# Kernel tuning notes

Hardware: AMD Instinct MI355X
Metric: run time of the kernel (lower is better)

Reference implementation:

```python
import jax, jax.numpy as jnp
import numpy as np
from jax import lax

N, CIN, COUT, H, W = 16, 512, 256, 32, 32
EPS = 1e-5


def _conv(x, w, b, pad_h, pad_w):
    # x: [N,Cin,H,W], w: [Cout,Cin,kh,kw], pad = ((top,bottom),(left,right))
    y = lax.conv_general_dilated(
        x, w, window_strides=(1, 1), padding=(pad_h, pad_w),
        dimension_numbers=("NCHW", "OIHW", "NCHW"))
    return y + b[None, :, None, None]


def setup_inputs() -> dict:
    key = jax.random.key(0)
    ks = jax.random.split(key, 12)
    s = 0.02
    return {
        "x": jax.random.normal(ks[0], (N, CIN, H, W), jnp.float32),
        "w1": jax.random.normal(ks[1], (COUT, CIN, 3, 3), jnp.float32) * s,
        "b1": jax.random.normal(ks[2], (COUT,), jnp.float32) * s,
        "w2": jax.random.normal(ks[3], (COUT, CIN, 2, 3), jnp.float32) * s,
        "b2": jax.random.normal(ks[4], (COUT,), jnp.float32) * s,
        "w3": jax.random.normal(ks[5], (COUT, CIN, 3, 2), jnp.float32) * s,
        "b3": jax.random.normal(ks[6], (COUT,), jnp.float32) * s,
        "w4": jax.random.normal(ks[7], (COUT, CIN, 2, 2), jnp.float32) * s,
        "b4": jax.random.normal(ks[8], (COUT,), jnp.float32) * s,
        "gamma": jnp.ones((COUT,), jnp.float32),
        "beta": jnp.zeros((COUT,), jnp.float32),
    }


def reference(x, w1, b1, w2, b2, w3, b3, w4, b4, gamma, beta):
    # torch F.pad(l,r,t,b) -> lax padding ((top,bottom),(left,right))
    o1 = _conv(x, w1, b1, (1, 1), (1, 1))  # 3x3, pad (1,1,1,1) -> [N,Cout,H,W]
    o2 = _conv(x, w2, b2, (1, 0), (1, 1))  # 2x3, pad (1,1,1,0)
    o3 = _conv(x, w3, b3, (1, 1), (1, 0))  # 3x2, pad (1,0,1,1)
    o4 = _conv(x, w4, b4, (1, 0), (1, 0))  # 2x2, pad (1,0,1,0)
    # pixel-shuffle interleave: o1->(even,even), o2->(odd,even), o3->(even,odd), o4->(odd,odd)
    row_even = jnp.stack([o1, o3], axis=-1).reshape(N, COUT, H, 2 * W)
    row_odd = jnp.stack([o2, o4], axis=-1).reshape(N, COUT, H, 2 * W)
    y = jnp.stack([row_even, row_odd], axis=-2).reshape(N, COUT, 2 * H, 2 * W)
    # BatchNorm2d, training mode: biased batch stats over (N,H,W)
    mean = jnp.mean(y, axis=(0, 2, 3), keepdims=True)
    var = jnp.mean(jnp.square(y - mean), axis=(0, 2, 3), keepdims=True)
    normed = (y - mean) * lax.rsqrt(var + EPS)
    normed = normed * gamma[None, :, None, None] + beta[None, :, None, None]
    return jax.nn.relu(normed)
```

## Files before the change

kernel.cpp:

```cpp
#include <hip/hip_runtime.h>
#include <hip/hip_bf16.h>


typedef unsigned short ushort_t;
typedef __attribute__((ext_vector_type(8))) short short8;
typedef __attribute__((ext_vector_type(4))) float floatx4;
typedef __attribute__((ext_vector_type(2))) float floatx2;
typedef __attribute__((ext_vector_type(4))) unsigned short u16x4;
typedef __attribute__((ext_vector_type(8))) unsigned short u16x8;
typedef __attribute__((ext_vector_type(4))) unsigned int u32x4;

#define XT_OFF    0u
#define WT_OFF    18939904u
#define BIAS_OFF  28377088u
#define STATS_OFF 28381184u

#define NSITES 204

#define ASYNC16(g, l) __builtin_amdgcn_global_load_lds( \
    (const __attribute__((address_space(1))) void*)(g), \
    (__attribute__((address_space(3))) void*)(l), 16, 0, 0)

__device__ __forceinline__ ushort_t f2bf(float f) {
  unsigned int u = __builtin_bit_cast(unsigned int, f);
  u += 0x7fffu + ((u >> 16) & 1u);
  return (ushort_t)(u >> 16);
}

__global__ __launch_bounds__(256) void prep_all(
    const float* __restrict__ x, ushort_t* __restrict__ xt,
    const float* __restrict__ w1, const float* __restrict__ w2,
    const float* __restrict__ w3, const float* __restrict__ w4,
    const float* __restrict__ b1, const float* __restrict__ b2,
    const float* __restrict__ b3, const float* __restrict__ b4,
    ushort_t* __restrict__ wt, float* __restrict__ bias,
    float* __restrict__ stats) {
  __shared__ ushort_t lds[128 * 36];
  const int t = threadIdx.x;
  if (blockIdx.x >= 544) {
    const int nout = blockIdx.x - 544;
    if (nout == 0 && t < 256) { stats[t] = 0.f; stats[256 + t] = 0.f; }
    const int q = nout >> 8, co = nout & 255;
    const int row = co * 4 + q;
    const float* wsrc; const float* bsrc; int khl, kwl;
    if (q == 0)      { wsrc = w1; bsrc = b1; khl = 3; kwl = 3; }
    else if (q == 1) { wsrc = w2; bsrc = b2; khl = 2; kwl = 3; }
    else if (q == 2) { wsrc = w3; bsrc = b3; khl = 3; kwl = 2; }
    else             { wsrc = w4; bsrc = b4; khl = 2; kwl = 2; }
    if (t == 0) bias[row] = bsrc[co];
    ushort_t* dst = wt + (size_t)row * 4608;
    for (int tap = 0; tap < 9; ++tap) {
      const int dh = tap / 3, dw = tap % 3;
      const bool valid = (dh < khl) && (dw < kwl);
#pragma unroll
      for (int cc = 0; cc < 2; ++cc) {
        const int ci = cc * 256 + t;
        ushort_t v = 0;
        if (valid)
          v = f2bf(wsrc[(((size_t)co * 512 + ci) * khl + dh) * kwl + dw]);
        dst[tap * 512 + ci] = v;
      }
    }
    return;
  }
  const int b = blockIdx.x;
  const int n = b / 34, hp = b % 34;
  ushort_t* dst = xt + (size_t)(n * 34 + hp) * (34 * 512);
  if (hp == 0 || hp == 33) {
    u32x4 z = {0u, 0u, 0u, 0u};
    for (int i = t; i < 2176; i += 256) ((u32x4*)dst)[i] = z;
    return;
  }
  const int h = hp - 1;
  {
    u32x4 z = {0u, 0u, 0u, 0u};
    if (t < 64) ((u32x4*)dst)[t] = z;
    else if (t < 128) ((u32x4*)(dst + 33 * 512))[t - 64] = z;
  }
  const size_t base = (size_t)n * 524288 + (size_t)h * 32;
  for (int ci0 = 0; ci0 < 512; ci0 += 128) {
    __syncthreads();
    {
      const int cil = t >> 3;
      const int w4 = (t & 7) << 2;
#pragma unroll
      for (int cc = 0; cc < 4; ++cc) {
        const int ci = cil + cc * 32;
        floatx4 v = *(const floatx4*)(x + base + (size_t)(ci0 + ci) * 1024 + w4);
        u16x4 hv;
#pragma unroll
        for (int j = 0; j < 4; ++j) hv[j] = f2bf(v[j]);
        *(u16x4*)&lds[ci * 36 + w4] = hv;
      }
    }
    __syncthreads();
    {
      const int w = t & 31;
      const int j8 = t >> 5;
#pragma unroll
      for (int cc2 = 0; cc2 < 2; ++cc2) {
        const int cil = cc2 * 64 + j8 * 8;
        u16x8 v;
#pragma unroll
        for (int j = 0; j < 8; ++j) v[j] = lds[(cil + j) * 36 + w];
        *(u16x8*)(dst + (w + 1) * 512 + ci0 + cil) = v;
      }
    }
  }
}

__global__ __launch_bounds__(256) void gemm_kernel(
    const ushort_t* __restrict__ xt, const ushort_t* __restrict__ wt,
    const float* __restrict__ bias, float* __restrict__ out,
    float* __restrict__ stats) {
  __shared__ char ldsX[NSITES * 128];
  __shared__ char ldsW[2][64 * 128];
  const int tid = threadIdx.x;
  const int bx = blockIdx.x;
  const int bn = bx & 15, bm = bx >> 4;
  const int n0 = bn << 6;
  const int n_img = bm >> 3;
  const int h0p = (bm & 7) << 2;
  const int wv = tid >> 6, lane = tid & 63;
  const int ri = lane & 15, kg = lane >> 4;
  const int wm = (wv & 1) << 6, wn = (wv >> 1) << 5;

  const char* xgp[7];
  char* xlp[7];
  {
    const char* xg = (const char*)(xt + (size_t)(n_img * 34 + h0p) * (34 * 512));
#pragma unroll
    for (int p = 0; p < 7; ++p) {
      const int idx = p * 256 + tid;
      const int site = idx >> 3, slot = idx & 7;
      const int c = slot ^ (site & 7);
      xgp[p] = xg + site * 1024 + (c << 4);
      xlp[p] = ldsX + idx * 16;
    }
  }
  const char* wgp[2];
  char* wlp0[2];
  char* wlp1[2];
#pragma unroll
  for (int p = 0; p < 2; ++p) {
    const int idx = p * 256 + tid;
    const int row = idx >> 3, slot = idx & 7;
    const int c = slot ^ (row & 7);
    wgp[p] = (const char*)wt + (size_t)(n0 + row) * 9216 + (c << 4);
    wlp0[p] = ldsW[0] + idx * 16;
    wlp1[p] = ldsW[1] + idx * 16;
  }

  floatx4 acc[2][4] = {};

  int arow[2], bsite[4];
#pragma unroll
  for (int f = 0; f < 2; ++f) arow[f] = wn + (f << 4) + ri;
#pragma unroll
  for (int fj = 0; fj < 4; ++fj)
    bsite[fj] = ((wm >> 5) + (fj >> 1)) * 34 + ((fj & 1) << 4) + ri;

  for (int chunk = 0; chunk < 8; ++chunk) {
    const int cb = chunk << 7;
#pragma unroll
    for (int p = 0; p < 6; ++p) ASYNC16(xgp[p] + cb, xlp[p]);
    if (tid < 96) ASYNC16(xgp[6] + cb, xlp[6]);
#pragma unroll
    for (int p = 0; p < 2; ++p) ASYNC16(wgp[p] + cb, wlp0[p]);
    __syncthreads();
#pragma unroll
    for (int tap = 0; tap < 9; ++tap) {
      if (tap < 8) {
        const int noff = ((tap + 1) << 10) + cb;
        if (tap & 1) {
#pragma unroll
          for (int p = 0; p < 2; ++p) ASYNC16(wgp[p] + noff, wlp0[p]);
        } else {
#pragma unroll
          for (int p = 0; p < 2; ++p) ASYNC16(wgp[p] + noff, wlp1[p]);
        }
      }
      const char* wb = ldsW[tap & 1];
      const int tapo = ((tap / 3) * 34 + (tap % 3)) * 128;
#pragma unroll
      for (int ks = 0; ks < 2; ++ks) {
        const int c = (ks << 2) + kg;
        short8 a4[2], b4[4];
#pragma unroll
        for (int f = 0; f < 2; ++f)
          a4[f] = *(const short8*)(wb + arow[f] * 128 +
                                   ((c ^ (arow[f] & 7)) << 4));
#pragma unroll
        for (int fj = 0; fj < 4; ++fj) {
          const int srow = bsite[fj] + (tap / 3) * 34 + (tap % 3);
          b4[fj] = *(const short8*)(ldsX + bsite[fj] * 128 + tapo +
                                    ((c ^ (srow & 7)) << 4));
        }
#pragma unroll
        for (int fi = 0; fi < 2; ++fi)
#pragma unroll
          for (int fj = 0; fj < 4; ++fj)
            acc[fi][fj] = __builtin_amdgcn_mfma_f32_16x16x32_bf16(
                a4[fi], b4[fj], acc[fi][fj], 0, 0, 0);
      }
      __syncthreads();
    }
  }

  const int quad = kg, colL = ri;
#pragma unroll
  for (int fi = 0; fi < 2; ++fi) {
    const int co = ((n0 + wn + (fi << 4)) >> 2) + quad;
    const floatx4 bv = *(const floatx4*)(bias + n0 + wn + (fi << 4) + (quad << 2));
    float s = 0.f, s2 = 0.f;
    float* obase = out + ((size_t)(n_img * 256 + co) << 12);
#pragma unroll
    for (int fj = 0; fj < 4; ++fj) {
      const int mb = wm + (fj << 4) + colL;
      const int hl = mb >> 5, w = mb & 31;
      const int h = h0p + hl;
      float v0 = acc[fi][fj][0] + bv[0];
      float v1 = acc[fi][fj][1] + bv[1];
      float v2 = acc[fi][fj][2] + bv[2];
      float v3 = acc[fi][fj][3] + bv[3];
      s += (v0 + v1) + (v2 + v3);
      s2 += v0 * v0 + v1 * v1 + v2 * v2 + v3 * v3;
      float* p = obase + (h << 7) + (w << 1);
      floatx2 e = {v0, v2};
      floatx2 o = {v1, v3};
      *(floatx2*)p = e;
      *(floatx2*)(p + 64) = o;
    }
#pragma unroll
    for (int off = 1; off < 16; off <<= 1) {
      s += __shfl_xor(s, off);
      s2 += __shfl_xor(s2, off);
    }
    if (colL == 0) {
      atomicAdd(&stats[co], s);
      atomicAdd(&stats[256 + co], s2);
    }
  }
}

__global__ __launch_bounds__(256) void bn_apply(
    float* __restrict__ y, const float* __restrict__ stats,
    const float* __restrict__ gamma, const float* __restrict__ beta) {
  const int b = blockIdx.x;
  const int co = b & 255;
  const int t = threadIdx.x;
  const float mean = stats[co] * (1.f / 65536.f);
  const float var = stats[256 + co] * (1.f / 65536.f) - mean * mean;
  const float rstd = rsqrtf(var + 1e-5f);
  const float scale = rstd * gamma[co];
  const float shift = beta[co] - mean * scale;
  float* p = y + (size_t)b * 4096;
#pragma unroll
  for (int it = 0; it < 4; ++it) {
    floatx4* q = (floatx4*)(p + (it * 256 + t) * 4);
    floatx4 v = *q;
#pragma unroll
    for (int e = 0; e < 4; ++e) v[e] = fmaxf(v[e] * scale + shift, 0.f);
    *q = v;
  }
}

extern "C" void kernel_launch(void* const* d_in, const int* in_sizes, int n_in,
                              void* d_out, int out_size, void* d_ws,
                              size_t ws_size, hipStream_t stream) {
  const float* x  = (const float*)d_in[0];
  const float* w1 = (const float*)d_in[1];
  const float* b1 = (const float*)d_in[2];
  const float* w2 = (const float*)d_in[3];
  const float* b2 = (const float*)d_in[4];
  const float* w3 = (const float*)d_in[5];
  const float* b3 = (const float*)d_in[6];
  const float* w4 = (const float*)d_in[7];
  const float* b4 = (const float*)d_in[8];
  const float* gamma = (const float*)d_in[9];
  const float* beta  = (const float*)d_in[10];
  float* out = (float*)d_out;

  char* ws = (char*)d_ws;
  ushort_t* xt   = (ushort_t*)(ws + XT_OFF);
  ushort_t* wt   = (ushort_t*)(ws + WT_OFF);
  float*    bias = (float*)(ws + BIAS_OFF);
  float*    st   = (float*)(ws + STATS_OFF);

  prep_all<<<544 + 1024, 256, 0, stream>>>(x, xt, w1, w2, w3, w4,
                                           b1, b2, b3, b4, wt, bias, st);
  gemm_kernel<<<2048, 256, 0, stream>>>(xt, wt, bias, out, st);
  bn_apply<<<4096, 256, 0, stream>>>(out, st, gamma, beta);
}
```

Measured before the change: 286.3 us.

## Load weights straight to registers in MFMA fragment layout and double N tile

The weight matrix is now pre-permuted into a panel layout that matches the MFMA A-fragment order. Each lane loads its fragments directly from global memory into a register double buffer, which removes the LDS staging of weights and the per-tap barrier. The block tile along N is doubled from 64 to 128, so each block holds a 4x4 fragment accumulator set and the grid is halved. This raises reuse of the staged X data, but it increases register pressure from 16 accumulators plus 16 u32x4 buffers, and it relies on global or L2 latency being hidden by prefetching one tap ahead.

```diff
diff --git a/kernel.cpp b/kernel.cpp
--- a/kernel.cpp
+++ b/kernel.cpp
@@ -16,6 +16,11 @@
 #define STATS_OFF 28381184u
 
 #define NSITES 204
+
+#define W_KS   8192
+#define W_TAP  16384
+#define W_CHK  147456
+#define W_PAN  1179648
 
 #define ASYNC16(g, l) __builtin_amdgcn_global_load_lds( \
     (const __attribute__((address_space(1))) void*)(g), \
@@ -42,13 +47,14 @@
     if (nout == 0 && t < 256) { stats[t] = 0.f; stats[256 + t] = 0.f; }
     const int q = nout >> 8, co = nout & 255;
     const int row = co * 4 + q;
+    const int panel = row >> 7, g = (row & 127) >> 4, riw = row & 15;
     const float* wsrc; const float* bsrc; int khl, kwl;
     if (q == 0)      { wsrc = w1; bsrc = b1; khl = 3; kwl = 3; }
     else if (q == 1) { wsrc = w2; bsrc = b2; khl = 2; kwl = 3; }
     else if (q == 2) { wsrc = w3; bsrc = b3; khl = 3; kwl = 2; }
     else             { wsrc = w4; bsrc = b4; khl = 2; kwl = 2; }
     if (t == 0) bias[row] = bsrc[co];
-    ushort_t* dst = wt + (size_t)row * 4608;
+    ushort_t* dstp = wt + (size_t)panel * (W_PAN / 2) + g * 512 + riw * 8;
     for (int tap = 0; tap < 9; ++tap) {
       const int dh = tap / 3, dw = tap % 3;
       const bool valid = (dh < khl) && (dw < kwl);
@@ -58,7 +64,10 @@
         ushort_t v = 0;
         if (valid)
           v = f2bf(wsrc[(((size_t)co * 512 + ci) * khl + dh) * kwl + dw]);
-        dst[tap * 512 + ci] = v;
+        const int chunk = ci >> 6, ks = (ci >> 5) & 1;
+        const int kg = (ci >> 3) & 3, e = ci & 7;
+        dstp[(size_t)chunk * (W_CHK / 2) + tap * (W_TAP / 2) +
+             ks * (W_KS / 2) + kg * 128 + e] = v;
       }
     }
     return;
@@ -114,16 +123,15 @@
     const float* __restrict__ bias, float* __restrict__ out,
     float* __restrict__ stats) {
   __shared__ char ldsX[NSITES * 128];
-  __shared__ char ldsW[2][64 * 128];
   const int tid = threadIdx.x;
   const int bx = blockIdx.x;
-  const int bn = bx & 15, bm = bx >> 4;
-  const int n0 = bn << 6;
+  const int bn = bx & 7, bm = bx >> 3;
+  const int n0 = bn << 7;
   const int n_img = bm >> 3;
   const int h0p = (bm & 7) << 2;
   const int wv = tid >> 6, lane = tid & 63;
   const int ri = lane & 15, kg = lane >> 4;
-  const int wm = (wv & 1) << 6, wn = (wv >> 1) << 5;
+  const int wm = (wv & 1) << 6, wn = (wv >> 1) << 6;
 
   const char* xgp[7];
   char* xlp[7];
@@ -138,78 +146,76 @@
       xlp[p] = ldsX + idx * 16;
     }
   }
-  const char* wgp[2];
-  char* wlp0[2];
-  char* wlp1[2];
-#pragma unroll
-  for (int p = 0; p < 2; ++p) {
-    const int idx = p * 256 + tid;
-    const int row = idx >> 3, slot = idx & 7;
-    const int c = slot ^ (row & 7);
-    wgp[p] = (const char*)wt + (size_t)(n0 + row) * 9216 + (c << 4);
-    wlp0[p] = ldsW[0] + idx * 16;
-    wlp1[p] = ldsW[1] + idx * 16;
-  }
-
-  floatx4 acc[2][4] = {};
-
-  int arow[2], bsite[4];
-#pragma unroll
-  for (int f = 0; f < 2; ++f) arow[f] = wn + (f << 4) + ri;
+
+  const char* wpan = (const char*)wt + (size_t)bn * W_PAN + (wn >> 4) * 1024 +
+                     lane * 16;
+
+  floatx4 acc[4][4] = {};
+  int bsite[4];
 #pragma unroll
   for (int fj = 0; fj < 4; ++fj)
     bsite[fj] = ((wm >> 5) + (fj >> 1)) * 34 + ((fj & 1) << 4) + ri;
 
+  u32x4 abuf[2][8];
+#pragma unroll
+  for (int k = 0; k < 2; ++k)
+#pragma unroll
+    for (int f = 0; f < 4; ++f)
+      abuf[0][k * 4 + f] = *(const u32x4*)(wpan + k * W_KS + f * 1024);
+
   for (int chunk = 0; chunk < 8; ++chunk) {
     const int cb = chunk << 7;
 #pragma unroll
     for (int p = 0; p < 6; ++p) ASYNC16(xgp[p] + cb, xlp[p]);
     if (tid < 96) ASYNC16(xgp[6] + cb, xlp[6]);
-#pragma unroll
-    for (int p = 0; p < 2; ++p) ASYNC16(wgp[p] + cb, wlp0[p]);
     __syncthreads();
 #pragma unroll
     for (int tap = 0; tap < 9; ++tap) {
-      if (tap < 8) {
-        const int noff = ((tap + 1) << 10) + cb;
-        if (tap & 1) {
-#pragma unroll
-          for (int p = 0; p < 2; ++p) ASYNC16(wgp[p] + noff, wlp0[p]);
-        } else {
-#pragma unroll
-          for (int p = 0; p < 2; ++p) ASYNC16(wgp[p] + noff, wlp1[p]);
-        }
-      }
-      const char* wb = ldsW[tap & 1];
-      const int tapo = ((tap / 3) * 34 + (tap % 3)) * 128;
+      if (tap < 8 || chunk < 7) {
+        const char* np = wpan +
+            ((tap < 8) ? ((size_t)chunk * W_CHK + (tap + 1) * W_TAP)
+                       : ((size_t)(chunk + 1) * W_CHK));
+#pragma unroll
+        for (int k = 0; k < 2; ++k)
+#pragma unroll
+          for (int f = 0; f < 4; ++f)
+            abuf[(tap + 1) & 1][k * 4 + f] =
+                *(const u32x4*)(np + k * W_KS + f * 1024);
+      }
+      const u32x4* ab = abuf[tap & 1];
+      const int tapsite = (tap / 3) * 34 + (tap % 3);
+      const int tapo = tapsite * 128;
 #pragma unroll
       for (int ks = 0; ks < 2; ++ks) {
         const int c = (ks << 2) + kg;
-        short8 a4[2], b4[4];
-#pragma unroll
-        for (int f = 0; f < 2; ++f)
-          a4[f] = *(const short8*)(wb + arow[f] * 128 +
-                                   ((c ^ (arow[f] & 7)) << 4));
+        short8 a4[4], b4[4];
+#pragma unroll
+        for (int f = 0; f < 4; ++f)
+          a4[f] = __builtin_bit_cast(short8, ab[ks * 4 + f]);
 #pragma unroll
         for (int fj = 0; fj < 4; ++fj) {
-          const int srow = bsite[fj] + (tap / 3) * 34 + (tap % 3);
+          const int srow = bsite[fj] + tapsite;
           b4[fj] = *(const short8*)(ldsX + bsite[fj] * 128 + tapo +
                                     ((c ^ (srow & 7)) << 4));
         }
 #pragma unroll
-        for (int fi = 0; fi < 2; ++fi)
+        for (int fi = 0; fi < 4; ++fi)
 #pragma unroll
           for (int fj = 0; fj < 4; ++fj)
             acc[fi][fj] = __builtin_amdgcn_mfma_f32_16x16x32_bf16(
                 a4[fi], b4[fj], acc[fi][fj], 0, 0, 0);
       }
-      __syncthreads();
-    }
+    }
+    if (chunk < 7) {
+#pragma unroll
+      for (int i = 0; i < 8; ++i) abuf[0][i] = abuf[1][i];
+    }
+    __syncthreads();
   }
 
   const int quad = kg, colL = ri;
 #pragma unroll
-  for (int fi = 0; fi < 2; ++fi) {
+  for (int fi = 0; fi < 4; ++fi) {
     const int co = ((n0 + wn + (fi << 4)) >> 2) + quad;
     const floatx4 bv = *(const floatx4*)(bias + n0 + wn + (fi << 4) + (quad << 2));
     float s = 0.f, s2 = 0.f;
@@ -289,6 +295,6 @@
 
   prep_all<<<544 + 1024, 256, 0, stream>>>(x, xt, w1, w2, w3, w4,
                                            b1, b2, b3, b4, wt, bias, st);
-  gemm_kernel<<<2048, 256, 0, stream>>>(xt, wt, bias, out, st);
+  gemm_kernel<<<1024, 256, 0, stream>>>(xt, wt, bias, out, st);
   bn_apply<<<4096, 256, 0, stream>>>(out, st, gamma, beta);
 }
```

Result: slower. 392.8 us (+37.2%).
